# Performance work log

Measured on AMD Instinct MI355X. Metric: run time of the kernel, lower is better.

Reference implementation:

```python
import jax, jax.numpy as jnp
import numpy as np

D_MODEL = 1024
N_HEADS = 16
HEAD_DIM = D_MODEL // N_HEADS


def setup_inputs() -> dict:
    key = jax.random.key(0)
    ks = jax.random.split(key, 5)
    B, T = 4, 2048
    x = jax.random.normal(ks[0], (B, T, D_MODEL), dtype=jnp.float32)
    s = 0.02
    W_qkv = jax.random.normal(ks[1], (D_MODEL, 3 * D_MODEL), dtype=jnp.float32) * s
    b_qkv = jnp.zeros((3 * D_MODEL,), dtype=jnp.float32)
    W_out = jax.random.normal(ks[2], (D_MODEL, D_MODEL), dtype=jnp.float32) * s
    b_out = jnp.zeros((D_MODEL,), dtype=jnp.float32)
    return {"x": x, "W_qkv": W_qkv, "b_qkv": b_qkv, "W_out": W_out, "b_out": b_out}


def reference(x, W_qkv, b_qkv, W_out, b_out):
    B, T, C = x.shape
    H, Dh = N_HEADS, HEAD_DIM
    qkv = x @ W_qkv + b_qkv                      # [B,T,3C]
    q, k, v = jnp.split(qkv, 3, axis=-1)
    q = q.reshape(B, T, H, Dh).transpose(0, 2, 1, 3)  # [B,H,T,Dh]
    k = k.reshape(B, T, H, Dh).transpose(0, 2, 1, 3)
    v = v.reshape(B, T, H, Dh).transpose(0, 2, 1, 3)
    scale = 1.0 / jnp.sqrt(jnp.float32(Dh))
    scores = jnp.einsum('bhqd,bhkd->bhqk', q, k) * scale  # [B,H,T,T]
    causal = jnp.tril(jnp.ones((T, T), dtype=bool))
    scores = jnp.where(causal[None, None], scores, jnp.float32(-jnp.inf))
    w = jax.nn.softmax(scores, axis=-1)
    y = jnp.einsum('bhqk,bhkd->bhqd', w, v)      # [B,H,T,Dh]
    y = y.transpose(0, 2, 1, 3).reshape(B, T, C)
    return y @ W_out + b_out
```

## Files before the change

### kernel.cpp

```cpp
#include <hip/hip_runtime.h>
#include <cstdint>
#include <math.h>

#define TT 2048
#define CC 1024
#define HH 16
#define DH 64
#define BB 4
#define MM 8192

typedef unsigned short u16;
typedef __bf16 bf16_t;
typedef bf16_t bf16x8 __attribute__((ext_vector_type(8)));
typedef float f32x4 __attribute__((ext_vector_type(4)));

static __device__ inline u16 f2bf(float f) {
    unsigned int u = __builtin_bit_cast(unsigned int, f);
    unsigned int lsb = (u >> 16) & 1u;
    u += 0x7fffu + lsb;
    return (u16)(u >> 16);
}

static __device__ inline unsigned int cvt_pk_bf16(float a, float b) {
    unsigned int r;
    asm volatile("v_cvt_pk_bf16_f32 %0, %1, %2" : "=v"(r) : "v"(a), "v"(b));
    return r;
}

#define GLL16(gptr, lptr)                                                            \
    __builtin_amdgcn_global_load_lds(                                                \
        (__attribute__((address_space(1))) void*)(gptr),                             \
        (__attribute__((address_space(3))) void*)(lptr), 16, 0, 0)

__global__ void __launch_bounds__(256)
prep_kernel(const float* __restrict__ x, u16* __restrict__ xb,
            const float* __restrict__ Wq, u16* __restrict__ wqt,
            const float* __restrict__ Wo, u16* __restrict__ wot) {
    const int bid = blockIdx.x;
    if (bid < 8192) {
        int i = bid * 256 + threadIdx.x;
        float4 v = ((const float4*)x)[i];
        uint2 o;
        o.x = cvt_pk_bf16(v.x, v.y);
        o.y = cvt_pk_bf16(v.z, v.w);
        ((uint2*)xb)[i] = o;
        return;
    }
    __shared__ u16 tile[32 * 34];
    const float* W; u16* Wt; int N, n0, k0;
    if (bid < 8192 + 3072) {
        int idx = bid - 8192;
        W = Wq; Wt = wqt; N = 3 * CC;
        n0 = (idx % 96) * 32; k0 = (idx / 96) * 32;
    } else {
        int idx = bid - 11264;
        W = Wo; Wt = wot; N = CC;
        n0 = (idx % 32) * 32; k0 = (idx / 32) * 32;
    }
    const int tx = threadIdx.x & 31;
    const int ty = threadIdx.x >> 5;
#pragma unroll
    for (int i = 0; i < 4; ++i) {
        int k = ty + i * 8;
        tile[tx * 34 + k] = f2bf(W[(size_t)(k0 + k) * N + n0 + tx]);
    }
    __syncthreads();
    const int tx2 = threadIdx.x & 15;
    const int ty2 = threadIdx.x >> 4;
#pragma unroll
    for (int i = 0; i < 2; ++i) {
        int r = ty2 + i * 16;
        *(unsigned int*)&Wt[(size_t)(n0 + r) * CC + k0 + 2 * tx2] =
            *(unsigned int*)&tile[r * 34 + 2 * tx2];
    }
}

template <int MODE>
__global__ void __launch_bounds__(256)
gemm_bt_kernel(const u16* __restrict__ A, const u16* __restrict__ Bt,
               const float* __restrict__ bias, float* __restrict__ Cout,
               u16* __restrict__ qws, u16* __restrict__ kws, u16* __restrict__ vtws,
               int Mdim, int Ndim, int Kdim) {
    __shared__ u16 As[2][128 * 32];
    __shared__ u16 Bs[2][128 * 32];

    const int tid  = threadIdx.x;
    const int w    = tid >> 6;
    const int lane = tid & 63;
    const int l15  = lane & 15;
    const int quad = lane >> 4;
    const int wm   = (w & 1) * 64;
    const int wn   = (w >> 1) * 64;
    const int m0   = blockIdx.y * 128;
    const int n0   = blockIdx.x * 128;

    const int row0  = tid >> 2;
    const int row1  = row0 + 64;
    const int colsw = (((tid & 3) ^ ((row0 >> 1) & 3))) << 3;

    f32x4 acc[4][4];
#pragma unroll
    for (int i = 0; i < 4; ++i)
#pragma unroll
        for (int j = 0; j < 4; ++j) acc[i][j] = (f32x4){0.f, 0.f, 0.f, 0.f};

    auto stageA = [&](int buf, int kc) {
        if (MODE == 0) {
            int kcc = kc + colsw, h = kcc >> 6, d = kcc & 63;
            int m = m0 + row0, b = m >> 11, t = m & 2047;
            GLL16(&A[(((size_t)(b * HH + h) * TT + t) * DH) + d], &As[buf][tid * 8]);
            m = m0 + row1; b = m >> 11; t = m & 2047;
            GLL16(&A[(((size_t)(b * HH + h) * TT + t) * DH) + d], &As[buf][(tid + 256) * 8]);
        } else {
            GLL16(&A[(size_t)(m0 + row0) * Kdim + kc + colsw], &As[buf][tid * 8]);
            GLL16(&A[(size_t)(m0 + row1) * Kdim + kc + colsw], &As[buf][(tid + 256) * 8]);
        }
    };

    stageA(0, 0);
    GLL16(&Bt[(size_t)(n0 + row0) * Kdim + colsw], &Bs[0][tid * 8]);
    GLL16(&Bt[(size_t)(n0 + row1) * Kdim + colsw], &Bs[0][(tid + 256) * 8]);

    const int csw = (quad ^ ((l15 >> 1) & 3)) * 8;

    const int nsteps = Kdim >> 5;
    for (int it = 0; it < nsteps; ++it) {
        const int buf = it & 1;
        __syncthreads();

        if (it + 1 < nsteps) {
            const int nbuf = buf ^ 1;
            const int kc = (it + 1) << 5;
            stageA(nbuf, kc);
            GLL16(&Bt[(size_t)(n0 + row0) * Kdim + kc + colsw], &Bs[nbuf][tid * 8]);
            GLL16(&Bt[(size_t)(n0 + row1) * Kdim + kc + colsw], &Bs[nbuf][(tid + 256) * 8]);
        }

        bf16x8 af[4], bfm[4];
#pragma unroll
        for (int mt = 0; mt < 4; ++mt)
            af[mt] = *(const bf16x8*)&As[buf][(wm + mt * 16 + l15) * 32 + csw];
#pragma unroll
        for (int nt = 0; nt < 4; ++nt)
            bfm[nt] = *(const bf16x8*)&Bs[buf][(wn + nt * 16 + l15) * 32 + csw];
#pragma unroll
        for (int mt = 0; mt < 4; ++mt)
#pragma unroll
            for (int nt = 0; nt < 4; ++nt)
                acc[mt][nt] = __builtin_amdgcn_mfma_f32_16x16x32_bf16(
                    af[mt], bfm[nt], acc[mt][nt], 0, 0, 0);
    }

#pragma unroll
    for (int mt = 0; mt < 4; ++mt) {
        int mrow_base = m0 + wm + mt * 16 + quad * 4;
#pragma unroll
        for (int nt = 0; nt < 4; ++nt) {
            int ncol = n0 + wn + nt * 16 + l15;
            float bv = bias[ncol];
            if (MODE == 0) {
#pragma unroll
                for (int r = 0; r < 4; ++r)
                    Cout[(size_t)(mrow_base + r) * Ndim + ncol] = acc[mt][nt][r] + bv;
            } else {
                int which = ncol >> 10, c = ncol & 1023;
                int h = c >> 6, d = c & 63;
                if (which == 2) {
                    int b = mrow_base >> 11, t = mrow_base & 2047;
                    int bh = b * HH + h;
                    int ch = (t >> 2) & 15;
                    int chp = (ch & 8) | (((ch >> 1) & 1) << 2) | ((ch & 1) << 1) | ((ch >> 2) & 1);
                    int tp = (t & ~63) | (chp << 2);
                    uint2 pv;
                    pv.x = cvt_pk_bf16(acc[mt][nt][0] + bv, acc[mt][nt][1] + bv);
                    pv.y = cvt_pk_bf16(acc[mt][nt][2] + bv, acc[mt][nt][3] + bv);
                    *(uint2*)&vtws[((size_t)bh * DH + d) * TT + tp] = pv;
                } else {
#pragma unroll
                    for (int r = 0; r < 4; ++r) {
                        int mrow = mrow_base + r;
                        int b = mrow >> 11, t = mrow & 2047;
                        int bh = b * HH + h;
                        float val = acc[mt][nt][r] + bv;
                        if (which == 0) {
                            qws[((size_t)bh * TT + t) * DH + d] = f2bf(val * 0.18033688f);
                        } else {
                            kws[((size_t)bh * TT + t) * DH + d] = f2bf(val);
                        }
                    }
                }
            }
        }
    }
}

__global__ void __launch_bounds__(256, 3)
attn_kernel(const u16* __restrict__ qws, const u16* __restrict__ kws,
            const u16* __restrict__ vtws, u16* __restrict__ yws) {
    __shared__ u16 Ks[2][64 * 68];
    __shared__ u16 Vs[2][64 * 68];

    const int tid  = threadIdx.x;
    const int w    = tid >> 6;
    const int lane = tid & 63;
    const int l15  = lane & 15;
    const int quad = lane >> 4;
    const int bh   = blockIdx.x;
    const int qt   = 15 - blockIdx.y;

    const u16* Kbase = kws + (size_t)bh * TT * DH;
    const u16* Vbase = vtws + (size_t)bh * DH * TT;

    const int srow  = tid >> 2;
    const int sc16  = (tid & 3) << 4;

    bf16x8 aones;
#pragma unroll
    for (int i = 0; i < 8; ++i) aones[i] = __builtin_bit_cast(bf16_t, (u16)0x3F80);

    const int q0     = qt * 128;
    const int qr0    = q0 + w * 32;
    const int ntiles = (q0 + 128) >> 6;

    const u16* Qp = qws + ((size_t)bh * TT + qr0) * DH;
    bf16x8 bqa[2], bqb[2];
#pragma unroll
    for (int kk = 0; kk < 2; ++kk) {
        bqa[kk] = *(const bf16x8*)&Qp[l15 * DH + kk * 32 + quad * 8];
        bqb[kk] = *(const bf16x8*)&Qp[(16 + l15) * DH + kk * 32 + quad * 8];
    }

    f32x4 o[2][4], ol[2];
#pragma unroll
    for (int qg = 0; qg < 2; ++qg) {
#pragma unroll
        for (int dt = 0; dt < 4; ++dt) o[qg][dt] = (f32x4){0.f, 0.f, 0.f, 0.f};
        ol[qg] = (f32x4){0.f, 0.f, 0.f, 0.f};
    }

    uint4 pk0 = *(const uint4*)&Kbase[(size_t)srow * DH + sc16];
    uint4 pk1 = *(const uint4*)&Kbase[(size_t)srow * DH + sc16 + 8];
    uint4 pv0 = *(const uint4*)&Vbase[(size_t)srow * TT + sc16];
    uint4 pv1 = *(const uint4*)&Vbase[(size_t)srow * TT + sc16 + 8];
    *(uint4*)&Ks[0][srow * 68 + sc16]     = pk0;
    *(uint4*)&Ks[0][srow * 68 + sc16 + 8] = pk1;
    *(uint4*)&Vs[0][srow * 68 + sc16]     = pv0;
    *(uint4*)&Vs[0][srow * 68 + sc16 + 8] = pv1;
    if (ntiles > 1) {
        pk0 = *(const uint4*)&Kbase[(size_t)(64 + srow) * DH + sc16];
        pk1 = *(const uint4*)&Kbase[(size_t)(64 + srow) * DH + sc16 + 8];
        pv0 = *(const uint4*)&Vbase[(size_t)srow * TT + 64 + sc16];
        pv1 = *(const uint4*)&Vbase[(size_t)srow * TT + 64 + sc16 + 8];
    }

    for (int it = 0; it < ntiles; ++it) {
        const int buf = it & 1;
        __syncthreads();

        if (it + 1 < ntiles) {
            *(uint4*)&Ks[buf ^ 1][srow * 68 + sc16]     = pk0;
            *(uint4*)&Ks[buf ^ 1][srow * 68 + sc16 + 8] = pk1;
            *(uint4*)&Vs[buf ^ 1][srow * 68 + sc16]     = pv0;
            *(uint4*)&Vs[buf ^ 1][srow * 68 + sc16 + 8] = pv1;
            if (it + 2 < ntiles) {
                int jn = (it + 2) << 6;
                pk0 = *(const uint4*)&Kbase[(size_t)(jn + srow) * DH + sc16];
                pk1 = *(const uint4*)&Kbase[(size_t)(jn + srow) * DH + sc16 + 8];
                pv0 = *(const uint4*)&Vbase[(size_t)srow * TT + jn + sc16];
                pv1 = *(const uint4*)&Vbase[(size_t)srow * TT + jn + sc16 + 8];
            }
        }

        const int j0 = it << 6;
        if (j0 > qr0 + 31) continue;

        bf16x8 ak[8];
#pragma unroll
        for (int kk = 0; kk < 2; ++kk)
#pragma unroll
            for (int kt = 0; kt < 4; ++kt)
                ak[kk * 4 + kt] =
                    *(const bf16x8*)&Ks[buf][(kt * 16 + l15) * 68 + kk * 32 + quad * 8];

        bf16x8 avr[8];
#pragma unroll
        for (int kk = 0; kk < 2; ++kk)
#pragma unroll
            for (int dt = 0; dt < 4; ++dt)
                avr[kk * 4 + dt] =
                    *(const bf16x8*)&Vs[buf][(dt * 16 + l15) * 68 + kk * 32 + quad * 8];

        f32x4 sa[4], sb[4];
#pragma unroll
        for (int kt = 0; kt < 4; ++kt) {
            sa[kt] = (f32x4){0.f, 0.f, 0.f, 0.f};
            sb[kt] = (f32x4){0.f, 0.f, 0.f, 0.f};
        }
#pragma unroll
        for (int kk = 0; kk < 2; ++kk)
#pragma unroll
            for (int kt = 0; kt < 4; ++kt)
                sa[kt] = __builtin_amdgcn_mfma_f32_16x16x32_bf16(ak[kk * 4 + kt], bqa[kk], sa[kt], 0, 0, 0);
#pragma unroll
        for (int kk = 0; kk < 2; ++kk)
#pragma unroll
            for (int kt = 0; kt < 4; ++kt)
                sb[kt] = __builtin_amdgcn_mfma_f32_16x16x32_bf16(ak[kk * 4 + kt], bqb[kk], sb[kt], 0, 0, 0);

        if (j0 + 63 > qr0) {
            int qy0 = qr0 + l15;
            int qy1 = qr0 + 16 + l15;
#pragma unroll
            for (int kt = 0; kt < 4; ++kt)
#pragma unroll
                for (int r = 0; r < 4; ++r) {
                    int key = j0 + kt * 16 + quad * 4 + r;
                    if (key > qy0) sa[kt][r] = -INFINITY;
                    if (key > qy1) sb[kt][r] = -INFINITY;
                }
        }

#pragma unroll
        for (int kt = 0; kt < 4; ++kt)
#pragma unroll
            for (int r = 0; r < 4; ++r) {
                sa[kt][r] = __builtin_amdgcn_exp2f(sa[kt][r]);
                sb[kt][r] = __builtin_amdgcn_exp2f(sb[kt][r]);
            }

        uint4 ua0, ua1, ub0, ub1;
        ua0.x = cvt_pk_bf16(sa[0][0], sa[0][1]);
        ua0.y = cvt_pk_bf16(sa[0][2], sa[0][3]);
        ua0.z = cvt_pk_bf16(sa[1][0], sa[1][1]);
        ua0.w = cvt_pk_bf16(sa[1][2], sa[1][3]);
        ua1.x = cvt_pk_bf16(sa[2][0], sa[2][1]);
        ua1.y = cvt_pk_bf16(sa[2][2], sa[2][3]);
        ua1.z = cvt_pk_bf16(sa[3][0], sa[3][1]);
        ua1.w = cvt_pk_bf16(sa[3][2], sa[3][3]);
        ub0.x = cvt_pk_bf16(sb[0][0], sb[0][1]);
        ub0.y = cvt_pk_bf16(sb[0][2], sb[0][3]);
        ub0.z = cvt_pk_bf16(sb[1][0], sb[1][1]);
        ub0.w = cvt_pk_bf16(sb[1][2], sb[1][3]);
        ub1.x = cvt_pk_bf16(sb[2][0], sb[2][1]);
        ub1.y = cvt_pk_bf16(sb[2][2], sb[2][3]);
        ub1.z = cvt_pk_bf16(sb[3][0], sb[3][1]);
        ub1.w = cvt_pk_bf16(sb[3][2], sb[3][3]);
        bf16x8 bpa0 = __builtin_bit_cast(bf16x8, ua0);
        bf16x8 bpa1 = __builtin_bit_cast(bf16x8, ua1);
        bf16x8 bpb0 = __builtin_bit_cast(bf16x8, ub0);
        bf16x8 bpb1 = __builtin_bit_cast(bf16x8, ub1);

#pragma unroll
        for (int dt = 0; dt < 4; ++dt)
            o[0][dt] = __builtin_amdgcn_mfma_f32_16x16x32_bf16(avr[dt], bpa0, o[0][dt], 0, 0, 0);
        ol[0] = __builtin_amdgcn_mfma_f32_16x16x32_bf16(aones, bpa0, ol[0], 0, 0, 0);
#pragma unroll
        for (int dt = 0; dt < 4; ++dt)
            o[0][dt] = __builtin_amdgcn_mfma_f32_16x16x32_bf16(avr[4 + dt], bpa1, o[0][dt], 0, 0, 0);
        ol[0] = __builtin_amdgcn_mfma_f32_16x16x32_bf16(aones, bpa1, ol[0], 0, 0, 0);
#pragma unroll
        for (int dt = 0; dt < 4; ++dt)
            o[1][dt] = __builtin_amdgcn_mfma_f32_16x16x32_bf16(avr[dt], bpb0, o[1][dt], 0, 0, 0);
        ol[1] = __builtin_amdgcn_mfma_f32_16x16x32_bf16(aones, bpb0, ol[1], 0, 0, 0);
#pragma unroll
        for (int dt = 0; dt < 4; ++dt)
            o[1][dt] = __builtin_amdgcn_mfma_f32_16x16x32_bf16(avr[4 + dt], bpb1, o[1][dt], 0, 0, 0);
        ol[1] = __builtin_amdgcn_mfma_f32_16x16x32_bf16(aones, bpb1, ol[1], 0, 0, 0);
    }

#pragma unroll
    for (int qg = 0; qg < 2; ++qg) {
        float rinv = __builtin_amdgcn_rcpf(ol[qg][0]);
        int t = qr0 + qg * 16 + l15;
#pragma unroll
        for (int dt = 0; dt < 4; ++dt) {
            uint2 yv;
            yv.x = cvt_pk_bf16(o[qg][dt][0] * rinv, o[qg][dt][1] * rinv);
            yv.y = cvt_pk_bf16(o[qg][dt][2] * rinv, o[qg][dt][3] * rinv);
            *(uint2*)&yws[((size_t)bh * TT + t) * DH + dt * 16 + quad * 4] = yv;
        }
    }
}


extern "C" void kernel_launch(void* const* d_in, const int* in_sizes, int n_in,
                              void* d_out, int out_size, void* d_ws, size_t ws_size,
                              hipStream_t stream) {
    const float* x     = (const float*)d_in[0];
    const float* W_qkv = (const float*)d_in[1];
    const float* b_qkv = (const float*)d_in[2];
    const float* W_out = (const float*)d_in[3];
    const float* b_out = (const float*)d_in[4];
    float* out = (float*)d_out;

    char* ws = (char*)d_ws;
    u16* xb   = (u16*)ws; ws += (size_t)MM * CC * 2;
    u16* wqt  = (u16*)ws; ws += (size_t)3 * CC * CC * 2;
    u16* wot  = (u16*)ws; ws += (size_t)CC * CC * 2;
    u16* qws  = (u16*)ws; ws += (size_t)MM * CC * 2;
    u16* kws  = (u16*)ws; ws += (size_t)MM * CC * 2;
    u16* vtws = (u16*)ws; ws += (size_t)MM * CC * 2;
    u16* yws  = (u16*)ws; ws += (size_t)MM * CC * 2;

    prep_kernel<<<8192 + 3072 + 1024, 256, 0, stream>>>(x, xb, W_qkv, wqt, W_out, wot);

    gemm_bt_kernel<1><<<dim3(24, 64), 256, 0, stream>>>(
        xb, wqt, b_qkv, nullptr, qws, kws, vtws, MM, 3 * CC, CC);

    attn_kernel<<<dim3(BB * HH, 16), 256, 0, stream>>>(qws, kws, vtws, yws);

    gemm_bt_kernel<0><<<dim3(8, 64), 256, 0, stream>>>(
        yws, wot, b_out, out, nullptr, nullptr, nullptr, MM, CC, CC);
}
```

Before: 233.7 us.

## Add 256x256-tile 512-thread QKV GEMM with swizzled direct-to-LDS pipelined loads

Replaces the generic 128x128-tile GEMM used for the QKV projection with a dedicated kernel. It uses 256x256 output tiles, 8 waves, a BK=64 step split into two 32-wide halves, and double-buffered direct global-to-LDS loads. The loads are interleaved with the MFMA quarter-steps, using an XOR swizzle and raised wave priority around the MFMAs. The aim is more operand reuse per LDS byte and better overlap of loads with matrix math. The cost is a 128KB LDS footprint, which limits occupancy to one block per CU, and only 384 blocks, which leaves a partial second wave.

```diff
diff --git a/kernel.cpp b/kernel.cpp
--- a/kernel.cpp
+++ b/kernel.cpp
@@ -72,6 +72,142 @@
         int r = ty2 + i * 16;
         *(unsigned int*)&Wt[(size_t)(n0 + r) * CC + k0 + 2 * tx2] =
             *(unsigned int*)&tile[r * 34 + 2 * tx2];
+    }
+}
+
+__global__ void __launch_bounds__(512, 2)
+gemm1_kernel(const u16* __restrict__ A, const u16* __restrict__ Bt,
+             const float* __restrict__ bias,
+             u16* __restrict__ qws, u16* __restrict__ kws, u16* __restrict__ vtws) {
+    __shared__ u16 lds[65536];
+
+    const int tid  = threadIdx.x;
+    const int w    = tid >> 6;
+    const int lane = tid & 63;
+    const int l15  = lane & 15;
+    const int quad = lane >> 4;
+    const int wm2  = w >> 2;
+    const int wn4  = w & 3;
+    const int m0   = blockIdx.y * 256;
+    const int n0   = blockIdx.x * 256;
+
+    const int csw  = (quad ^ ((l15 >> 1) & 3)) * 8;
+
+    const int srow = tid >> 2;
+    const int sgp  = tid & 3;
+    const int sgl  = (sgp ^ ((srow >> 1) & 3)) * 8;
+
+    f32x4 acc[8][4];
+#pragma unroll
+    for (int i = 0; i < 8; ++i)
+#pragma unroll
+        for (int j = 0; j < 4; ++j) acc[i][j] = (f32x4){0.f, 0.f, 0.f, 0.f};
+
+    auto stA = [&](int buf, int kh, int kt) {
+#pragma unroll
+        for (int j = 0; j < 2; ++j) {
+            int row = j * 128 + srow;
+            GLL16(&A[(size_t)(m0 + row) * CC + kt * 64 + kh * 32 + sgl],
+                  &lds[(size_t)(buf * 2 + kh) * 8192 + (j * 512 + tid) * 8]);
+        }
+    };
+    auto stB = [&](int buf, int kh, int kt) {
+#pragma unroll
+        for (int j = 0; j < 2; ++j) {
+            int row = j * 128 + srow;
+            GLL16(&Bt[(size_t)(n0 + row) * CC + kt * 64 + kh * 32 + sgl],
+                  &lds[32768 + (size_t)(buf * 2 + kh) * 8192 + (j * 512 + tid) * 8]);
+        }
+    };
+
+    const int ntiles = CC / 64;
+    stA(0, 0, 0); stB(0, 0, 0);
+    __builtin_amdgcn_sched_barrier(0);
+    stA(0, 1, 0); stB(0, 1, 0);
+
+    for (int t = 0; t < ntiles; ++t) {
+        const int buf  = t & 1;
+        const int nbuf = buf ^ 1;
+        const bool more = (t + 1 < ntiles);
+
+#pragma unroll
+        for (int q = 0; q < 4; ++q) {
+            const int kk = q >> 1;
+            const int mq = q & 1;
+
+            if (q == 0) {
+                asm volatile("s_waitcnt vmcnt(4)" ::: "memory");
+                __builtin_amdgcn_s_barrier();
+                __builtin_amdgcn_sched_barrier(0);
+            } else if (q == 2) {
+                if (more) asm volatile("s_waitcnt vmcnt(4)" ::: "memory");
+                else      asm volatile("s_waitcnt vmcnt(0)" ::: "memory");
+                __builtin_amdgcn_s_barrier();
+                __builtin_amdgcn_sched_barrier(0);
+            }
+
+            if (more) {
+                if      (q == 0) stA(nbuf, 0, t + 1);
+                else if (q == 1) stB(nbuf, 0, t + 1);
+                else if (q == 2) stA(nbuf, 1, t + 1);
+                else             stB(nbuf, 1, t + 1);
+            }
+
+            bf16x8 af[4], bfm[4];
+            const int abase = (buf * 2 + kk) * 8192;
+            const int bbase = 32768 + (buf * 2 + kk) * 8192;
+#pragma unroll
+            for (int i = 0; i < 4; ++i)
+                af[i] = *(const bf16x8*)&lds[abase + (wm2 * 128 + (mq * 4 + i) * 16 + l15) * 32 + csw];
+#pragma unroll
+            for (int nt = 0; nt < 4; ++nt)
+                bfm[nt] = *(const bf16x8*)&lds[bbase + (wn4 * 64 + nt * 16 + l15) * 32 + csw];
+
+            __builtin_amdgcn_s_setprio(1);
+#pragma unroll
+            for (int i = 0; i < 4; ++i)
+#pragma unroll
+                for (int nt = 0; nt < 4; ++nt)
+                    acc[mq * 4 + i][nt] = __builtin_amdgcn_mfma_f32_16x16x32_bf16(
+                        af[i], bfm[nt], acc[mq * 4 + i][nt], 0, 0, 0);
+            __builtin_amdgcn_s_setprio(0);
+        }
+    }
+
+#pragma unroll
+    for (int mt = 0; mt < 8; ++mt) {
+        int mrow_base = m0 + wm2 * 128 + mt * 16 + quad * 4;
+#pragma unroll
+        for (int nt = 0; nt < 4; ++nt) {
+            int ncol = n0 + wn4 * 64 + nt * 16 + l15;
+            float bv = bias[ncol];
+            int which = ncol >> 10, c = ncol & 1023;
+            int h = c >> 6, d = c & 63;
+            if (which == 2) {
+                int b = mrow_base >> 11, t = mrow_base & 2047;
+                int bh = b * HH + h;
+                int ch = (t >> 2) & 15;
+                int chp = (ch & 8) | (((ch >> 1) & 1) << 2) | ((ch & 1) << 1) | ((ch >> 2) & 1);
+                int tp = (t & ~63) | (chp << 2);
+                uint2 pv;
+                pv.x = cvt_pk_bf16(acc[mt][nt][0] + bv, acc[mt][nt][1] + bv);
+                pv.y = cvt_pk_bf16(acc[mt][nt][2] + bv, acc[mt][nt][3] + bv);
+                *(uint2*)&vtws[((size_t)bh * DH + d) * TT + tp] = pv;
+            } else {
+#pragma unroll
+                for (int r = 0; r < 4; ++r) {
+                    int mrow = mrow_base + r;
+                    int b = mrow >> 11, t = mrow & 2047;
+                    int bh = b * HH + h;
+                    float val = acc[mt][nt][r] + bv;
+                    if (which == 0) {
+                        qws[((size_t)bh * TT + t) * DH + d] = f2bf(val * 0.18033688f);
+                    } else {
+                        kws[((size_t)bh * TT + t) * DH + d] = f2bf(val);
+                    }
+                }
+            }
+        }
     }
 }
 
@@ -404,8 +540,7 @@
 
     prep_kernel<<<8192 + 3072 + 1024, 256, 0, stream>>>(x, xb, W_qkv, wqt, W_out, wot);
 
-    gemm_bt_kernel<1><<<dim3(24, 64), 256, 0, stream>>>(
-        xb, wqt, b_qkv, nullptr, qws, kws, vtws, MM, 3 * CC, CC);
+    gemm1_kernel<<<dim3(12, 32), 512, 0, stream>>>(xb, wqt, b_qkv, qws, kws, vtws);
 
     attn_kernel<<<dim3(BB * HH, 16), 256, 0, stream>>>(qws, kws, vtws, yws);
 
```

Measured after the change: 232.9 us. No clear change (-0.4%).
